# Performance work log

Measured on AMD Instinct MI355X. Metric: run time of the kernel, lower is better.

## Reference

```python
import jax, jax.numpy as jnp
import numpy as np

B, T, F, H = 8192, 256, 64, 50

def setup_inputs() -> dict:
    key = jax.random.key(0)
    ks = jax.random.split(key, 6)
    s = 0.1
    x = jax.random.normal(ks[0], (B, T, F), dtype=jnp.float32)
    W = jax.random.normal(ks[1], (F, 3 * H), dtype=jnp.float32) * s   # input kernel [z|r|h]
    U = jax.random.normal(ks[2], (H, 3 * H), dtype=jnp.float32) * s   # recurrent kernel
    b = jax.random.normal(ks[3], (2, 3 * H), dtype=jnp.float32) * s   # [input bias; recurrent bias] (reset_after=True)
    Wd = jax.random.normal(ks[4], (H, 1), dtype=jnp.float32) * s
    bd = jax.random.normal(ks[5], (1,), dtype=jnp.float32) * s
    return {"x": x, "W": W, "U": U, "b": b, "Wd": Wd, "bd": bd}

def _gru_last_hidden(x, W, U, b):
    # Precompute input projections for all timesteps: [B,T,3H]
    xp = jnp.einsum('btf,fg->btg', x, W) + b[0]
    xp = jnp.transpose(xp, (1, 0, 2))  # [T,B,3H] for scan over time
    bi = b[1]

    def step(h, xt):
        rp = h @ U + bi                       # recurrent projection [B,3H]
        xz, xr, xh = jnp.split(xt, 3, axis=-1)
        rz, rr, rh = jnp.split(rp, 3, axis=-1)
        z = jax.nn.sigmoid(xz + rz)
        r = jax.nn.sigmoid(xr + rr)
        hh = jnp.tanh(xh + r * rh)            # reset_after=True formulation
        h_new = z * h + (1.0 - z) * hh
        return h_new, None

    h0 = jnp.zeros((x.shape[0], U.shape[0]), dtype=x.dtype)
    h_last, _ = jax.lax.scan(step, h0, xp)
    return h_last

def reference(x, W, U, b, Wd, bd):
    h = _gru_last_hidden(x, W, U, b)   # [B,H]
    # Dropout is identity at inference time
    return h @ Wd + bd                 # [B,1]
```

## Files before the change

kernel.cpp:

```cpp
#include <hip/hip_runtime.h>


typedef __attribute__((ext_vector_type(8))) short s16x8;
typedef __attribute__((ext_vector_type(4))) float f32x4;

#define T_STEPS 256
#define F_IN    64
#define GW      212

__device__ __forceinline__ unsigned short f2bf(float f) {
  unsigned int u = __builtin_bit_cast(unsigned int, f);
  u += 0x7FFFu + ((u >> 16) & 1u);
  return (unsigned short)(u >> 16);
}

__global__ __launch_bounds__(256, 2) void gru_fused(
    const float* __restrict__ x,  const float* __restrict__ W,
    const float* __restrict__ U,  const float* __restrict__ b,
    const float* __restrict__ Wd, const float* __restrict__ bdp,
    float* __restrict__ out)
{
  __shared__ __align__(16) unsigned short Abuf[2048];
  __shared__ float G[16 * GW];
  __shared__ float bzs[64], brs[64], bh0[64], bh1[64];

  const int tid  = threadIdx.x;
  const int l    = tid & 63;
  const int w    = tid >> 6;
  const int lhi  = l >> 4, llo = l & 15;
  const int row0 = blockIdx.x << 4;

  if (tid < 50) {
    bzs[tid] = b[tid]        + b[150 + tid];
    brs[tid] = b[50 + tid]   + b[200 + tid];
    bh0[tid] = b[100 + tid];
    bh1[tid] = b[250 + tid];
  }
  ((unsigned long long*)Abuf)[256 + tid] = 0ULL;

  s16x8 breg[3][4];
  #pragma unroll
  for (int wi = 0; wi < 3; ++wi) {
    const int nt  = w * 3 + wi;
    const int col = nt * 16 + llo;
    #pragma unroll
    for (int kc = 0; kc < 4; ++kc) {
      s16x8 f;
      #pragma unroll
      for (int i = 0; i < 8; ++i) {
        const int k = kc * 32 + lhi * 8 + i;
        float v = 0.f;
        if (col < 150 && k < 114)
          v = (k < 64) ? W[k * 150 + col] : U[(k - 64) * 150 + col];
        f[i] = (short)f2bf(v);
      }
      breg[wi][kc] = f;
    }
  }

  const float* xlane =
      x + ((long)(row0 + llo) * T_STEPS) * F_IN + (w & 1) * 32 + lhi * 8;
  f32x4 xa = {0.f,0.f,0.f,0.f}, xb = xa;
  if (w < 2) {
    xa = *(const f32x4*)(xlane + 0);
    xb = *(const f32x4*)(xlane + 4);
  }
  if (w < 2) {
    s16x8 f;
    f[0]=(short)f2bf(xa[0]); f[1]=(short)f2bf(xa[1]);
    f[2]=(short)f2bf(xa[2]); f[3]=(short)f2bf(xa[3]);
    f[4]=(short)f2bf(xb[0]); f[5]=(short)f2bf(xb[1]);
    f[6]=(short)f2bf(xb[2]); f[7]=(short)f2bf(xb[3]);
    *(s16x8*)((char*)Abuf + w * 1024 + l * 16) = f;
  }
  __syncthreads();

  float h0 = 0.f, h1 = 0.f, h2 = 0.f, h3 = 0.f;
  const int rowg = tid >> 4;
  const int jg   = tid & 15;

  for (int t = 0; t < T_STEPS; ++t) {
    int t1 = t + 1; if (t1 >= T_STEPS) t1 = T_STEPS - 1;
    if (w < 2) {
      const float* p = xlane + (long)t1 * F_IN;
      xa = *(const f32x4*)p;
      xb = *(const f32x4*)(p + 4);
    }

    const char* Ab = (const char*)Abuf;
    s16x8 a0 = *(const s16x8*)(Ab +    0 + l * 16);
    s16x8 a1 = *(const s16x8*)(Ab + 1024 + l * 16);
    s16x8 a2 = *(const s16x8*)(Ab + 2048 + l * 16);
    s16x8 a3 = *(const s16x8*)(Ab + 3072 + l * 16);

    f32x4 lo[3], hi[3];
    #pragma unroll
    for (int wi = 0; wi < 3; ++wi) {
      f32x4 zlo = {0.f,0.f,0.f,0.f};
      zlo    = __builtin_amdgcn_mfma_f32_16x16x32_bf16(a0, breg[wi][0], zlo, 0,0,0);
      lo[wi] = __builtin_amdgcn_mfma_f32_16x16x32_bf16(a1, breg[wi][1], zlo, 0,0,0);
      f32x4 zhi = {0.f,0.f,0.f,0.f};
      zhi    = __builtin_amdgcn_mfma_f32_16x16x32_bf16(a2, breg[wi][2], zhi, 0,0,0);
      hi[wi] = __builtin_amdgcn_mfma_f32_16x16x32_bf16(a3, breg[wi][3], zhi, 0,0,0);
    }

    #pragma unroll
    for (int wi = 0; wi < 3; ++wi) {
      const int nt = w * 3 + wi;
      if (nt < 10) {
        const int col = nt * 16 + llo;
        #pragma unroll
        for (int r = 0; r < 4; ++r) {
          const int row = lhi * 4 + r;
          const float vlo = lo[wi][r], vhi = hi[wi][r];
          G[row * GW + col] = (col < 100) ? (vlo + vhi) : vlo;
          if (col >= 100 && col < 150) G[row * GW + col + 60] = vhi;
        }
      }
    }
    __syncthreads();

    if (w < 2) {
      s16x8 f;
      f[0]=(short)f2bf(xa[0]); f[1]=(short)f2bf(xa[1]);
      f[2]=(short)f2bf(xa[2]); f[3]=(short)f2bf(xa[3]);
      f[4]=(short)f2bf(xb[0]); f[5]=(short)f2bf(xb[1]);
      f[6]=(short)f2bf(xb[2]); f[7]=(short)f2bf(xb[3]);
      *(s16x8*)((char*)Abuf + w * 1024 + l * 16) = f;
    }

    #pragma unroll
    for (int i = 0; i < 4; ++i) {
      if (i < 3 || jg < 2) {
        const int j = jg + 16 * i;
        const float* Gr = &G[rowg * GW];
        const float zs = Gr[j], rs = Gr[j + 50], xh = Gr[j + 100], rh = Gr[j + 160];
        const float z = __builtin_amdgcn_rcpf(1.f + __expf(-(zs + bzs[j])));
        const float r = __builtin_amdgcn_rcpf(1.f + __expf(-(rs + brs[j])));
        const float e = __expf(2.f * (xh + bh0[j] + r * (rh + bh1[j])));
        const float hh = 1.f - 2.f * __builtin_amdgcn_rcpf(1.f + e);
        const float hp = (i == 0) ? h0 : (i == 1) ? h1 : (i == 2) ? h2 : h3;
        const float hn = z * hp + (1.f - z) * hh;
        if (i == 0) h0 = hn; else if (i == 1) h1 = hn;
        else if (i == 2) h2 = hn; else h3 = hn;
        const int k = 64 + j, kc = k >> 5, kk = k & 31;
        Abuf[kc * 512 + ((kk >> 3) * 16 + rowg) * 8 + (kk & 7)] = f2bf(hn);
      }
    }
    __syncthreads();
  }

  float p = h0 * Wd[jg] + h1 * Wd[jg + 16] + h2 * Wd[jg + 32];
  if (jg < 2) p += h3 * Wd[jg + 48];
  p += __shfl_xor(p, 1);
  p += __shfl_xor(p, 2);
  p += __shfl_xor(p, 4);
  p += __shfl_xor(p, 8);
  if (jg == 0) out[row0 + rowg] = p + bdp[0];
}

extern "C" void kernel_launch(void* const* d_in, const int* in_sizes, int n_in,
                              void* d_out, int out_size, void* d_ws, size_t ws_size,
                              hipStream_t stream) {
  const float* x   = (const float*)d_in[0];
  const float* W   = (const float*)d_in[1];
  const float* U   = (const float*)d_in[2];
  const float* b   = (const float*)d_in[3];
  const float* Wd  = (const float*)d_in[4];
  const float* bdp = (const float*)d_in[5];
  float* out = (float*)d_out;
  gru_fused<<<dim3(512), dim3(256), 0, stream>>>(x, W, U, b, Wd, bdp, out);
}
```

Baseline: 871.3 us.

## Align MFMA output columns with gate units to drop the shared gate scratch

Each wave now owns 16 hidden units and computes the z, r and h gate columns for those same units. The gate nonlinearities can then be applied straight from the MFMA accumulators, so the shared G buffer and one of the two barriers per timestep go away. The x and h MFMA operands are double-buffered in shared memory, every thread helps stage x, and x is prefetched two steps ahead. The cost is wasted MFMA lanes, since units 50-63 are padding, and a more involved index layout for the h writes.

```diff
diff --git a/kernel.cpp b/kernel.cpp
--- a/kernel.cpp
+++ b/kernel.cpp
@@ -1,17 +1,15 @@
 #include <hip/hip_runtime.h>
+#include <hip/hip_bf16.h>
 
 
 typedef __attribute__((ext_vector_type(8))) short s16x8;
+typedef __attribute__((ext_vector_type(4))) short s16x4;
 typedef __attribute__((ext_vector_type(4))) float f32x4;
 
-#define T_STEPS 256
-#define F_IN    64
-#define GW      212
+#define TS 256
 
 __device__ __forceinline__ unsigned short f2bf(float f) {
-  unsigned int u = __builtin_bit_cast(unsigned int, f);
-  u += 0x7FFFu + ((u >> 16) & 1u);
-  return (unsigned short)(u >> 16);
+  return __builtin_bit_cast(unsigned short, __float2bfloat16(f));
 }
 
 __global__ __launch_bounds__(256, 2) void gru_fused(
@@ -20,29 +18,31 @@
     const float* __restrict__ Wd, const float* __restrict__ bdp,
     float* __restrict__ out)
 {
-  __shared__ __align__(16) unsigned short Abuf[2048];
-  __shared__ float G[16 * GW];
-  __shared__ float bzs[64], brs[64], bh0[64], bh1[64];
+  __shared__ __align__(16) unsigned short xbuf[2][2][512];
+  __shared__ __align__(16) unsigned short hbuf[2][2][512];
+  __shared__ float red[4][16];
 
-  const int tid  = threadIdx.x;
-  const int l    = tid & 63;
-  const int w    = tid >> 6;
-  const int lhi  = l >> 4, llo = l & 15;
+  const int tid = threadIdx.x;
+  const int l   = tid & 63;
+  const int w   = tid >> 6;
+  const int lhi = l >> 4, llo = l & 15;
   const int row0 = blockIdx.x << 4;
+  const int u = (w << 4) + llo;
 
-  if (tid < 50) {
-    bzs[tid] = b[tid]        + b[150 + tid];
-    brs[tid] = b[50 + tid]   + b[200 + tid];
-    bh0[tid] = b[100 + tid];
-    bh1[tid] = b[250 + tid];
+  ((unsigned long long*)hbuf)[tid]       = 0ULL;
+  ((unsigned long long*)hbuf)[tid + 256] = 0ULL;
+
+  float bz = 0.f, br = 0.f, bh0 = 0.f, bh1 = 0.f;
+  if (u < 50) {
+    bz  = b[u]       + b[150 + u];
+    br  = b[50 + u]  + b[200 + u];
+    bh0 = b[100 + u];
+    bh1 = b[250 + u];
   }
-  ((unsigned long long*)Abuf)[256 + tid] = 0ULL;
 
   s16x8 breg[3][4];
   #pragma unroll
-  for (int wi = 0; wi < 3; ++wi) {
-    const int nt  = w * 3 + wi;
-    const int col = nt * 16 + llo;
+  for (int g = 0; g < 3; ++g) {
     #pragma unroll
     for (int kc = 0; kc < 4; ++kc) {
       s16x8 f;
@@ -50,113 +50,104 @@
       for (int i = 0; i < 8; ++i) {
         const int k = kc * 32 + lhi * 8 + i;
         float v = 0.f;
-        if (col < 150 && k < 114)
-          v = (k < 64) ? W[k * 150 + col] : U[(k - 64) * 150 + col];
+        if (u < 50 && k < 114)
+          v = (k < 64) ? W[k * 150 + g * 50 + u]
+                       : U[(k - 64) * 150 + g * 50 + u];
         f[i] = (short)f2bf(v);
       }
-      breg[wi][kc] = f;
+      breg[g][kc] = f;
     }
   }
 
-  const float* xlane =
-      x + ((long)(row0 + llo) * T_STEPS) * F_IN + (w & 1) * 32 + lhi * 8;
-  f32x4 xa = {0.f,0.f,0.f,0.f}, xb = xa;
-  if (w < 2) {
-    xa = *(const f32x4*)(xlane + 0);
-    xb = *(const f32x4*)(xlane + 4);
+  const int sc    = tid >> 7;
+  const int sla   = (tid >> 1) & 63;
+  const int shalf = tid & 1;
+  const float* xp = x + (long)(row0 + (sla & 15)) * (TS * 64)
+                      + sc * 32 + (sla >> 4) * 8 + shalf * 4;
+  unsigned short* const xdst0 = &xbuf[0][sc][sla * 8 + shalf * 4];
+  unsigned short* const xdst1 = &xbuf[1][sc][sla * 8 + shalf * 4];
+
+  f32x4 xc = *(const f32x4*)xp;
+  {
+    s16x4 pk;
+    pk[0] = (short)f2bf(xc[0]); pk[1] = (short)f2bf(xc[1]);
+    pk[2] = (short)f2bf(xc[2]); pk[3] = (short)f2bf(xc[3]);
+    *(s16x4*)xdst0 = pk;
   }
-  if (w < 2) {
-    s16x8 f;
-    f[0]=(short)f2bf(xa[0]); f[1]=(short)f2bf(xa[1]);
-    f[2]=(short)f2bf(xa[2]); f[3]=(short)f2bf(xa[3]);
-    f[4]=(short)f2bf(xb[0]); f[5]=(short)f2bf(xb[1]);
-    f[6]=(short)f2bf(xb[2]); f[7]=(short)f2bf(xb[3]);
-    *(s16x8*)((char*)Abuf + w * 1024 + l * 16) = f;
-  }
+  xc = *(const f32x4*)(xp + 64);
   __syncthreads();
 
   float h0 = 0.f, h1 = 0.f, h2 = 0.f, h3 = 0.f;
-  const int rowg = tid >> 4;
-  const int jg   = tid & 15;
+  f32x4 xn;
 
-  for (int t = 0; t < T_STEPS; ++t) {
-    int t1 = t + 1; if (t1 >= T_STEPS) t1 = T_STEPS - 1;
-    if (w < 2) {
-      const float* p = xlane + (long)t1 * F_IN;
-      xa = *(const f32x4*)p;
-      xb = *(const f32x4*)(p + 4);
-    }
-
-    const char* Ab = (const char*)Abuf;
-    s16x8 a0 = *(const s16x8*)(Ab +    0 + l * 16);
-    s16x8 a1 = *(const s16x8*)(Ab + 1024 + l * 16);
-    s16x8 a2 = *(const s16x8*)(Ab + 2048 + l * 16);
-    s16x8 a3 = *(const s16x8*)(Ab + 3072 + l * 16);
-
-    f32x4 lo[3], hi[3];
-    #pragma unroll
-    for (int wi = 0; wi < 3; ++wi) {
-      f32x4 zlo = {0.f,0.f,0.f,0.f};
-      zlo    = __builtin_amdgcn_mfma_f32_16x16x32_bf16(a0, breg[wi][0], zlo, 0,0,0);
-      lo[wi] = __builtin_amdgcn_mfma_f32_16x16x32_bf16(a1, breg[wi][1], zlo, 0,0,0);
-      f32x4 zhi = {0.f,0.f,0.f,0.f};
-      zhi    = __builtin_amdgcn_mfma_f32_16x16x32_bf16(a2, breg[wi][2], zhi, 0,0,0);
-      hi[wi] = __builtin_amdgcn_mfma_f32_16x16x32_bf16(a3, breg[wi][3], zhi, 0,0,0);
-    }
-
-    #pragma unroll
-    for (int wi = 0; wi < 3; ++wi) {
-      const int nt = w * 3 + wi;
-      if (nt < 10) {
-        const int col = nt * 16 + llo;
-        #pragma unroll
-        for (int r = 0; r < 4; ++r) {
-          const int row = lhi * 4 + r;
-          const float vlo = lo[wi][r], vhi = hi[wi][r];
-          G[row * GW + col] = (col < 100) ? (vlo + vhi) : vlo;
-          if (col >= 100 && col < 150) G[row * GW + col + 60] = vhi;
-        }
-      }
-    }
-    __syncthreads();
-
-    if (w < 2) {
-      s16x8 f;
-      f[0]=(short)f2bf(xa[0]); f[1]=(short)f2bf(xa[1]);
-      f[2]=(short)f2bf(xa[2]); f[3]=(short)f2bf(xa[3]);
-      f[4]=(short)f2bf(xb[0]); f[5]=(short)f2bf(xb[1]);
-      f[6]=(short)f2bf(xb[2]); f[7]=(short)f2bf(xb[3]);
-      *(s16x8*)((char*)Abuf + w * 1024 + l * 16) = f;
-    }
-
-    #pragma unroll
-    for (int i = 0; i < 4; ++i) {
-      if (i < 3 || jg < 2) {
-        const int j = jg + 16 * i;
-        const float* Gr = &G[rowg * GW];
-        const float zs = Gr[j], rs = Gr[j + 50], xh = Gr[j + 100], rh = Gr[j + 160];
-        const float z = __builtin_amdgcn_rcpf(1.f + __expf(-(zs + bzs[j])));
-        const float r = __builtin_amdgcn_rcpf(1.f + __expf(-(rs + brs[j])));
-        const float e = __expf(2.f * (xh + bh0[j] + r * (rh + bh1[j])));
-        const float hh = 1.f - 2.f * __builtin_amdgcn_rcpf(1.f + e);
-        const float hp = (i == 0) ? h0 : (i == 1) ? h1 : (i == 2) ? h2 : h3;
-        const float hn = z * hp + (1.f - z) * hh;
-        if (i == 0) h0 = hn; else if (i == 1) h1 = hn;
-        else if (i == 2) h2 = hn; else h3 = hn;
-        const int k = 64 + j, kc = k >> 5, kk = k & 31;
-        Abuf[kc * 512 + ((kk >> 3) * 16 + rowg) * 8 + (kk & 7)] = f2bf(hn);
-      }
-    }
-    __syncthreads();
+#define GRU_STEP(T, XC, XN, PR, PW, XDST)                                      \
+  {                                                                            \
+    int tpre = (T) + 2; if (tpre > TS - 1) tpre = TS - 1;                      \
+    XN = *(const f32x4*)(xp + (long)tpre * 64);                                \
+    const s16x8 a0 = *(const s16x8*)&xbuf[PR][0][l * 8];                       \
+    const s16x8 a1 = *(const s16x8*)&xbuf[PR][1][l * 8];                       \
+    const s16x8 a2 = *(const s16x8*)&hbuf[PR][0][l * 8];                       \
+    const s16x8 a3 = *(const s16x8*)&hbuf[PR][1][l * 8];                       \
+    f32x4 lo[3], hi[3];                                                        \
+    _Pragma("unroll")                                                          \
+    for (int g = 0; g < 3; ++g) {                                              \
+      f32x4 zz = {0.f, 0.f, 0.f, 0.f};                                         \
+      zz    = __builtin_amdgcn_mfma_f32_16x16x32_bf16(a2, breg[g][2], zz, 0,0,0);\
+      hi[g] = __builtin_amdgcn_mfma_f32_16x16x32_bf16(a3, breg[g][3], zz, 0,0,0);\
+      f32x4 yy = {0.f, 0.f, 0.f, 0.f};                                         \
+      yy    = __builtin_amdgcn_mfma_f32_16x16x32_bf16(a0, breg[g][0], yy, 0,0,0);\
+      lo[g] = __builtin_amdgcn_mfma_f32_16x16x32_bf16(a1, breg[g][1], yy, 0,0,0);\
+    }                                                                          \
+    {                                                                          \
+      s16x4 pk;                                                                \
+      pk[0] = (short)f2bf(XC[0]); pk[1] = (short)f2bf(XC[1]);                  \
+      pk[2] = (short)f2bf(XC[2]); pk[3] = (short)f2bf(XC[3]);                  \
+      *(s16x4*)(XDST) = pk;                                                    \
+    }                                                                          \
+    _Pragma("unroll")                                                          \
+    for (int r = 0; r < 4; ++r) {                                              \
+      float hv = (r == 0) ? h0 : (r == 1) ? h1 : (r == 2) ? h2 : h3;           \
+      const float zs = lo[0][r] + hi[0][r] + bz;                               \
+      const float rs = lo[1][r] + hi[1][r] + br;                               \
+      const float z  = __builtin_amdgcn_rcpf(1.f + __expf(-zs));               \
+      const float rr = __builtin_amdgcn_rcpf(1.f + __expf(-rs));               \
+      const float ar = lo[2][r] + bh0 + rr * (hi[2][r] + bh1);                 \
+      const float e  = __expf(2.f * ar);                                       \
+      const float hh = 1.f - 2.f * __builtin_amdgcn_rcpf(1.f + e);             \
+      hv = hh + z * (hv - hh);                                                 \
+      if (r == 0) h0 = hv; else if (r == 1) h1 = hv;                           \
+      else if (r == 2) h2 = hv; else h3 = hv;                                  \
+      hbuf[PW][u >> 5][(((u & 31) >> 3) * 16 + lhi * 4 + r) * 8 + (u & 7)] =   \
+          f2bf(hv);                                                            \
+    }                                                                          \
+    __syncthreads();                                                           \
   }
 
-  float p = h0 * Wd[jg] + h1 * Wd[jg + 16] + h2 * Wd[jg + 32];
-  if (jg < 2) p += h3 * Wd[jg + 48];
-  p += __shfl_xor(p, 1);
-  p += __shfl_xor(p, 2);
-  p += __shfl_xor(p, 4);
-  p += __shfl_xor(p, 8);
-  if (jg == 0) out[row0 + rowg] = p + bdp[0];
+  for (int t = 0; t < TS; t += 2) {
+    GRU_STEP(t,     xc, xn, 0, 1, xdst1)
+    GRU_STEP(t + 1, xn, xc, 1, 0, xdst0)
+  }
+#undef GRU_STEP
+
+  const float Wdv = (u < 50) ? Wd[u] : 0.f;
+  float p0 = h0 * Wdv, p1 = h1 * Wdv, p2 = h2 * Wdv, p3 = h3 * Wdv;
+  #pragma unroll
+  for (int m = 1; m < 16; m <<= 1) {
+    p0 += __shfl_xor(p0, m);
+    p1 += __shfl_xor(p1, m);
+    p2 += __shfl_xor(p2, m);
+    p3 += __shfl_xor(p3, m);
+  }
+  if (llo == 0) {
+    red[w][lhi * 4 + 0] = p0;
+    red[w][lhi * 4 + 1] = p1;
+    red[w][lhi * 4 + 2] = p2;
+    red[w][lhi * 4 + 3] = p3;
+  }
+  __syncthreads();
+  if (tid < 16)
+    out[row0 + tid] =
+        red[0][tid] + red[1][tid] + red[2][tid] + red[3][tid] + bdp[0];
 }
 
 extern "C" void kernel_launch(void* const* d_in, const int* in_sizes, int n_in,
```

Result: faster. 827.5 us (-5.0%).
